# Kernel optimization log

Hardware: AMD Instinct MI355X
Metric: run time of the kernel (lower is better)

The kernel has to match this reference:

```python
import jax, jax.numpy as jnp
import numpy as np

DIM = 1024
H = 16
HD = DIM // H
SCALE = HD ** -0.5
EPS = 1e-5


def setup_inputs() -> dict:
    key = jax.random.key(0)
    ks = jax.random.split(key, 12)
    B, S = 4, 1024
    s = 0.02
    return {
        "image_feat": jax.random.normal(ks[0], (B, S, DIM), jnp.float32),
        "waveform_feat": jax.random.normal(ks[1], (B, S, DIM), jnp.float32),
        "Wq_i": jax.random.normal(ks[2], (DIM, DIM), jnp.float32) * s,
        "bq_i": jnp.zeros((DIM,), jnp.float32),
        "Wkv_w": jax.random.normal(ks[3], (DIM, 2 * DIM), jnp.float32) * s,
        "bkv_w": jnp.zeros((2 * DIM,), jnp.float32),
        "Wq_w": jax.random.normal(ks[4], (DIM, DIM), jnp.float32) * s,
        "bq_w": jnp.zeros((DIM,), jnp.float32),
        "Wkv_i": jax.random.normal(ks[5], (DIM, 2 * DIM), jnp.float32) * s,
        "bkv_i": jnp.zeros((2 * DIM,), jnp.float32),
        "Wp": jax.random.normal(ks[6], (2 * DIM, DIM), jnp.float32) * s,
        "bp": jnp.zeros((DIM,), jnp.float32),
        "gamma": jnp.ones((DIM,), jnp.float32),
        "beta": jnp.zeros((DIM,), jnp.float32),
    }


def _heads(x, B, S):
    # (B, S, DIM) -> (B, H, S, HD)
    return x.reshape(B, S, H, HD).transpose(0, 2, 1, 3)


def _cross_attn(q, k, v, clamp):
    # q,k,v: (B, H, S, HD)
    scores = jnp.einsum("bhqd,bhkd->bhqk", q, k) * SCALE
    if clamp:
        scores = jnp.clip(scores, -100.0, 100.0)
    attn = jax.nn.softmax(scores, axis=-1)
    return jnp.einsum("bhqk,bhkd->bhqd", attn, v)


def reference(image_feat, waveform_feat, Wq_i, bq_i, Wkv_w, bkv_w,
              Wq_w, bq_w, Wkv_i, bkv_i, Wp, bp, gamma, beta):
    B, S, _ = image_feat.shape
    # image queries attend to waveform K/V (with clamp)
    q_s = _heads(image_feat @ Wq_i + bq_i, B, S)
    kv_f = (waveform_feat @ Wkv_w + bkv_w).reshape(B, S, 2, H, HD)
    k_f = kv_f[:, :, 0].transpose(0, 2, 1, 3)
    v_f = kv_f[:, :, 1].transpose(0, 2, 1, 3)
    img_att = _cross_attn(q_s, k_f, v_f, clamp=True)
    img_att = img_att.transpose(0, 2, 1, 3).reshape(B, S, DIM)
    # waveform queries attend to image K/V (no clamp, as in source)
    q_f = _heads(waveform_feat @ Wq_w + bq_w, B, S)
    kv_s = (image_feat @ Wkv_i + bkv_i).reshape(B, S, 2, H, HD)
    k_s = kv_s[:, :, 0].transpose(0, 2, 1, 3)
    v_s = kv_s[:, :, 1].transpose(0, 2, 1, 3)
    wav_att = _cross_attn(q_f, k_s, v_s, clamp=False)
    wav_att = wav_att.transpose(0, 2, 1, 3).reshape(B, S, DIM)
    fused = jnp.concatenate([img_att, wav_att], axis=-1)
    out = fused @ Wp + bp
    # LayerNorm over last dim
    mu = jnp.mean(out, axis=-1, keepdims=True)
    var = jnp.var(out, axis=-1, keepdims=True)
    out = (out - mu) * jax.lax.rsqrt(var + EPS) * gamma + beta
    return out
```

## Files before the change

### kernel.cpp

```cpp
#include <hip/hip_runtime.h>
#include <hip/hip_bf16.h>

#define DEVINL __device__ __forceinline__

typedef float f32x4 __attribute__((ext_vector_type(4)));
typedef __bf16 bf16x8 __attribute__((ext_vector_type(8)));

DEVINL void gld_lds16(const void* g, void* l) {
  __builtin_amdgcn_global_load_lds(
      (const __attribute__((address_space(1))) unsigned int*)g,
      (__attribute__((address_space(3))) unsigned int*)l, 16, 0, 0);
}

DEVINL unsigned short f2bf(float f) {
  __bf16 h = (__bf16)f;
  return __builtin_bit_cast(unsigned short, h);
}

DEVINL f32x4 mfma16(bf16x8 a, bf16x8 b, f32x4 c) {
  return __builtin_amdgcn_mfma_f32_16x16x32_bf16(a, b, c, 0, 0, 0);
}

DEVINL void swz3(int& bn, int& bm, int& z) {
  int gx = gridDim.x, gy = gridDim.y;
  int nwg = gx * gy * gridDim.z;
  int flat = blockIdx.x + gx * (blockIdx.y + gy * blockIdx.z);
  int wg = (flat & 7) * (nwg >> 3) + (flat >> 3);
  bn = wg % gx;
  int t = wg / gx;
  bm = t % gy;
  z = t / gy;
}

__global__ __launch_bounds__(256) void cvt2_kernel(const float* __restrict__ inA,
                                                   unsigned short* __restrict__ outA,
                                                   const float* __restrict__ inB,
                                                   unsigned short* __restrict__ outB) {
  int bx = blockIdx.x;
  const float* in = bx < 4096 ? inA : inB;
  unsigned short* outp = bx < 4096 ? outA : outB;
  int i = (bx & 4095) * 256 + threadIdx.x;
  float4 v = ((const float4*)in)[i];
  ushort4 o;
  o.x = f2bf(v.x); o.y = f2bf(v.y); o.z = f2bf(v.z); o.w = f2bf(v.w);
  ((ushort4*)outp)[i] = o;
}

struct TransArgs {
  const float* W[5];
  unsigned short* Wt[5];
};

DEVINL void trans_tile(const float* W, unsigned short* Wt, int K, int N,
                       int xt, int yt) {
  __shared__ float t[32][33];
  int n0 = xt * 32, k0 = yt * 32;
  int tx = threadIdx.x & 31, ty = threadIdx.x >> 5;
#pragma unroll
  for (int i = 0; i < 4; i++)
    t[ty + i * 8][tx] = W[(size_t)(k0 + ty + i * 8) * N + n0 + tx];
  __syncthreads();
#pragma unroll
  for (int i = 0; i < 4; i++) {
    int n = ty + i * 8;
    Wt[(size_t)(n0 + n) * K + k0 + tx] = f2bf(t[tx][n]);
  }
}

__global__ __launch_bounds__(256) void transpose_all(TransArgs a) {
  int t = blockIdx.x;
  if (t < 1024)       trans_tile(a.W[0], a.Wt[0], 1024, 1024, t % 32, t / 32);
  else if (t < 3072)  { int l = t - 1024; trans_tile(a.W[1], a.Wt[1], 1024, 2048, l % 64, l / 64); }
  else if (t < 4096)  { int l = t - 3072; trans_tile(a.W[2], a.Wt[2], 1024, 1024, l % 32, l / 32); }
  else if (t < 6144)  { int l = t - 4096; trans_tile(a.W[3], a.Wt[3], 1024, 2048, l % 64, l / 64); }
  else                { int l = t - 6144; trans_tile(a.W[4], a.Wt[4], 2048, 1024, l % 32, l / 32); }
}

template <int BM, int BN, int MREP, int NREP>
DEVINL void g256_main(const unsigned short* A, const unsigned short* Bt, int K,
                      int bm, int bn, unsigned short* Al, unsigned short* Bl,
                      f32x4 (&acc)[MREP][NREP]) {
  const int tid = threadIdx.x;
  const int wave = tid >> 6, lane = tid & 63;
  const int lr = lane & 15;
  const int lk16 = (lane >> 4) * 16;
  const int wm = wave >> 2, wn = wave & 3;
  const int swz = (lr & 7) << 4;
  const int nk = K >> 6;
  const size_t Kb = (size_t)K * 2;

#pragma unroll
  for (int m = 0; m < MREP; m++)
#pragma unroll
    for (int n = 0; n < NREP; n++) acc[m][n] = f32x4{0.f, 0.f, 0.f, 0.f};

  auto stage = [&](int buf, int kt) {
#pragma unroll
    for (int i = 0; i < BM / 64; i++) {
      int chunk = i * 512 + tid;
      int row = chunk >> 3, cb = (chunk & 7) * 16;
      const char* src = (const char*)A + (size_t)(bm * BM + row) * Kb +
                        kt * 128 + (cb ^ ((row & 7) << 4));
      char* dst = (char*)(Al + (size_t)buf * BM * 64) + (i * 512 + wave * 64) * 16;
      gld_lds16(src, dst);
    }
#pragma unroll
    for (int i = 0; i < BN / 64; i++) {
      int chunk = i * 512 + tid;
      int row = chunk >> 3, cb = (chunk & 7) * 16;
      const char* src = (const char*)Bt + (size_t)(bn * BN + row) * Kb +
                        kt * 128 + (cb ^ ((row & 7) << 4));
      char* dst = (char*)(Bl + (size_t)buf * BN * 64) + (i * 512 + wave * 64) * 16;
      gld_lds16(src, dst);
    }
  };

  stage(0, 0);
  for (int kt = 0; kt < nk; ++kt) {
    __syncthreads();
    if (kt + 1 < nk) stage((kt + 1) & 1, kt + 1);
    const char* ab = (const char*)(Al + (size_t)(kt & 1) * BM * 64);
    const char* bb = (const char*)(Bl + (size_t)(kt & 1) * BN * 64);
#pragma unroll
    for (int kk = 0; kk < 2; kk++) {
      bf16x8 af[MREP], bf[NREP];
#pragma unroll
      for (int m = 0; m < MREP; m++) {
        int row = wm * (BM / 2) + m * 16 + lr;
        af[m] = *(const bf16x8*)(ab + row * 128 + ((kk * 64 + lk16) ^ swz));
      }
#pragma unroll
      for (int n = 0; n < NREP; n++) {
        int row = wn * (BN / 4) + n * 16 + lr;
        bf[n] = *(const bf16x8*)(bb + row * 128 + ((kk * 64 + lk16) ^ swz));
      }
#pragma unroll
      for (int m = 0; m < MREP; m++)
#pragma unroll
        for (int n = 0; n < NREP; n++)
          acc[m][n] = mfma16(af[m], bf[n], acc[m][n]);
    }
  }
}

__global__ __launch_bounds__(512, 2) void gemm_q2(const unsigned short* __restrict__ A0,
                                                  const unsigned short* __restrict__ B0,
                                                  const float* __restrict__ bias0,
                                                  unsigned short* __restrict__ C0,
                                                  const unsigned short* __restrict__ A1,
                                                  const unsigned short* __restrict__ B1,
                                                  const float* __restrict__ bias1,
                                                  unsigned short* __restrict__ C1) {
  __shared__ unsigned short Al[2 * 256 * 64];
  __shared__ unsigned short Bl[2 * 128 * 64];
  int bn, bm, z;
  swz3(bn, bm, z);
  const unsigned short* A = z ? A1 : A0;
  const unsigned short* Bt = z ? B1 : B0;
  const float* bias = z ? bias1 : bias0;
  unsigned short* C = z ? C1 : C0;
  const int lane = threadIdx.x & 63, wave = threadIdx.x >> 6;
  const int lr = lane & 15, g4 = lane >> 4;
  const int wm = wave >> 2, wn = wave & 3;
  f32x4 acc[8][2];
  g256_main<256, 128, 8, 2>(A, Bt, 1024, bm, bn, Al, Bl, acc);
#pragma unroll
  for (int n = 0; n < 2; n++) {
    int col = bn * 128 + wn * 32 + n * 16 + lr;
    float bv = bias[col];
#pragma unroll
    for (int m = 0; m < 8; m++) {
      int row0 = bm * 256 + wm * 128 + m * 16 + g4 * 4;
#pragma unroll
      for (int r = 0; r < 4; r++)
        C[(size_t)(row0 + r) * 1024 + col] = f2bf((acc[m][n][r] + bv) * 0.125f);
    }
  }
}

__global__ __launch_bounds__(512, 4) void gemm_kv2(const unsigned short* __restrict__ A0,
                                                   const unsigned short* __restrict__ B0,
                                                   const float* __restrict__ bias0,
                                                   unsigned short* __restrict__ K0,
                                                   unsigned short* __restrict__ V0,
                                                   const unsigned short* __restrict__ A1,
                                                   const unsigned short* __restrict__ B1,
                                                   const float* __restrict__ bias1,
                                                   unsigned short* __restrict__ K1,
                                                   unsigned short* __restrict__ V1) {
  __shared__ unsigned short Al[2 * 128 * 64];
  __shared__ unsigned short Bl[2 * 128 * 64];
  int bn, bm, z;
  swz3(bn, bm, z);
  const unsigned short* A = z ? A1 : A0;
  const unsigned short* Bt = z ? B1 : B0;
  const float* bias = z ? bias1 : bias0;
  unsigned short* Kbuf = z ? K1 : K0;
  unsigned short* VtG = z ? V1 : V0;
  const int lane = threadIdx.x & 63, wave = threadIdx.x >> 6;
  const int lr = lane & 15, g4 = lane >> 4;
  const int wm = wave >> 2, wn = wave & 3;
  f32x4 acc[4][2];
  g256_main<128, 128, 4, 2>(A, Bt, 1024, bm, bn, Al, Bl, acc);
#pragma unroll
  for (int n = 0; n < 2; n++) {
    int col = bn * 128 + wn * 32 + n * 16 + lr;
    float bv = bias[col];
#pragma unroll
    for (int m = 0; m < 4; m++) {
      int row0 = bm * 128 + wm * 64 + m * 16 + g4 * 4;
      if (col < 1024) {
#pragma unroll
        for (int r = 0; r < 4; r++)
          Kbuf[(size_t)(row0 + r) * 1024 + col] = f2bf(acc[m][n][r] + bv);
      } else {
        int h = (col - 1024) >> 6, d = (col - 1024) & 63;
        int b = row0 >> 10, s = row0 & 1023;
        ushort4 pk;
        pk.x = f2bf(acc[m][n][0] + bv);
        pk.y = f2bf(acc[m][n][1] + bv);
        pk.z = f2bf(acc[m][n][2] + bv);
        pk.w = f2bf(acc[m][n][3] + bv);
        *(ushort4*)&VtG[((size_t)(b * 16 + h) * 64 + d) * 1024 + s] = pk;
      }
    }
  }
}

__global__ __launch_bounds__(512, 4) void gemm_out(const unsigned short* __restrict__ A,
                                                   const unsigned short* __restrict__ Bt,
                                                   const float* __restrict__ bias,
                                                   float* __restrict__ C) {
  __shared__ unsigned short Al[2 * 128 * 64];
  __shared__ unsigned short Bl[2 * 128 * 64];
  int bn, bm, z;
  swz3(bn, bm, z);
  const int lane = threadIdx.x & 63, wave = threadIdx.x >> 6;
  const int lr = lane & 15, g4 = lane >> 4;
  const int wm = wave >> 2, wn = wave & 3;
  f32x4 acc[4][2];
  g256_main<128, 128, 4, 2>(A, Bt, 2048, bm, bn, Al, Bl, acc);
#pragma unroll
  for (int n = 0; n < 2; n++) {
    int col = bn * 128 + wn * 32 + n * 16 + lr;
    float bv = bias[col];
#pragma unroll
    for (int m = 0; m < 4; m++) {
      int row0 = bm * 128 + wm * 64 + m * 16 + g4 * 4;
#pragma unroll
      for (int r = 0; r < 4; r++)
        C[(size_t)(row0 + r) * 1024 + col] = acc[m][n][r] + bv;
    }
  }
  (void)z;
}

__global__ __launch_bounds__(256, 4) void attn_fused(const unsigned short* __restrict__ Qs,
                                                     const unsigned short* __restrict__ Ks,
                                                     const unsigned short* __restrict__ Vs,
                                                     const unsigned short* __restrict__ Qf,
                                                     const unsigned short* __restrict__ Kf,
                                                     const unsigned short* __restrict__ Vf,
                                                     unsigned short* __restrict__ Out) {
  __shared__ unsigned short Kl[2][64 * 64];
  __shared__ unsigned short Vt[2][64 * 64];
  __shared__ unsigned short Pl[4][16 * 64];

  const int tid = threadIdx.x;
  const int wave = tid >> 6, lane = tid & 63;
  const int qt = blockIdx.y & 7;
  const int u = blockIdx.x + (blockIdx.y >> 3) * 16;
  const int dir = u >> 6, bh = u & 63;
  const int b = bh >> 4, h = bh & 15;
  const unsigned short* Q = dir ? Qf : Qs;
  const unsigned short* Kg = dir ? Kf : Ks;
  const unsigned short* VtG = dir ? Vf : Vs;
  const int outColBase = dir ? 1024 : 0;
  const bool doClamp = (dir == 0);

  const int q16 = lane & 15;
  const int g4 = lane >> 4;
  const int lk16 = g4 * 16;

  bf16x8 qa[2][2];
#pragma unroll
  for (int g = 0; g < 2; g++) {
    const size_t qrow = (size_t)b * 1024 + qt * 128 + wave * 32 + g * 16 + q16;
    const char* qp = (const char*)(Q + qrow * 1024 + h * 64);
    qa[g][0] = *(const bf16x8*)(qp + lk16);
    qa[g][1] = *(const bf16x8*)(qp + 64 + lk16);
  }

  f32x4 acc[2][4] = {};
  float mrun[2] = {-1e30f, -1e30f}, lsum[2] = {0.f, 0.f};

  const char* kbase = (const char*)Kg + (size_t)b * 1024 * 2048 + h * 128;
  const char* vbase = (const char*)VtG + (size_t)bh * 64 * 2048;

  auto stage = [&](int buf, int kt) {
#pragma unroll
    for (int p2 = 0; p2 < 2; p2++) {
      int chunk = tid + p2 * 256;
      int r = chunk >> 3, cb = (chunk & 7) * 16;
      const char* src = kbase + (size_t)(kt * 64 + r) * 2048 + (cb ^ ((r & 7) << 4));
      char* dst = (char*)&Kl[buf][0] + (p2 * 256 + wave * 64) * 16;
      gld_lds16(src, dst);
    }
#pragma unroll
    for (int p2 = 0; p2 < 2; p2++) {
      int chunk = tid + p2 * 256;
      int d = chunk >> 3, ko = (chunk & 7) * 16;
      const char* src = vbase + (size_t)d * 2048 + kt * 128 + (ko ^ ((d & 7) << 4));
      char* dst = (char*)&Vt[buf][0] + (p2 * 256 + wave * 64) * 16;
      gld_lds16(src, dst);
    }
  };

  char* pb = (char*)&Pl[wave][0];

  stage(0, 0);
  for (int kt = 0; kt < 16; ++kt) {
    __syncthreads();
    if (kt < 15) stage((kt + 1) & 1, kt + 1);
    const char* kb = (const char*)&Kl[kt & 1][0];
    const char* vb = (const char*)&Vt[kt & 1][0];

#pragma unroll
    for (int g = 0; g < 2; g++) {
      f32x4 st[4];
#pragma unroll
      for (int t4 = 0; t4 < 4; t4++) {
        int krow = t4 * 16 + q16;
        int sw = (krow & 7) << 4;
        const char* kr = kb + krow * 128;
        bf16x8 kb0 = *(const bf16x8*)(kr + ((0 + lk16) ^ sw));
        bf16x8 kb1 = *(const bf16x8*)(kr + ((64 + lk16) ^ sw));
        f32x4 s = {};
        s = mfma16(kb0, qa[g][0], s);
        s = mfma16(kb1, qa[g][1], s);
        if (doClamp) {
#pragma unroll
          for (int r = 0; r < 4; r++)
            s[r] = fminf(fmaxf(s[r], -100.f), 100.f);
        }
        st[t4] = s;
      }

      float mx = fmaxf(fmaxf(fmaxf(st[0][0], st[0][1]), fmaxf(st[0][2], st[0][3])),
                       fmaxf(fmaxf(st[1][0], st[1][1]), fmaxf(st[1][2], st[1][3])));
      float mx2 = fmaxf(fmaxf(fmaxf(st[2][0], st[2][1]), fmaxf(st[2][2], st[2][3])),
                        fmaxf(fmaxf(st[3][0], st[3][1]), fmaxf(st[3][2], st[3][3])));
      mx = fmaxf(mx, mx2);
      mx = fmaxf(mx, __shfl_xor(mx, 16, 64));
      mx = fmaxf(mx, __shfl_xor(mx, 32, 64));

      if (!__all(mx <= mrun[g] + 8.f)) {
        float mnew = fmaxf(mrun[g], mx);
        float al = __expf(mrun[g] - mnew);
        mrun[g] = mnew;
        lsum[g] *= al;
        float alr[4];
#pragma unroll
        for (int r = 0; r < 4; r++) alr[r] = __shfl(al, 4 * g4 + r, 64);
#pragma unroll
        for (int n = 0; n < 4; n++)
#pragma unroll
          for (int r = 0; r < 4; r++) acc[g][n][r] *= alr[r];
      }
      const float m = mrun[g];
      float sum = 0.f;
#pragma unroll
      for (int t4 = 0; t4 < 4; t4++) {
#pragma unroll
        for (int r = 0; r < 4; r++) {
          float pv = __expf(st[t4][r] - m);
          st[t4][r] = pv;
          sum += pv;
        }
      }
      sum += __shfl_xor(sum, 16, 64);
      sum += __shfl_xor(sum, 32, 64);
      lsum[g] += sum;

#pragma unroll
      for (int t4 = 0; t4 < 4; t4++) {
        unsigned plo = ((unsigned)f2bf(st[t4][1]) << 16) | f2bf(st[t4][0]);
        unsigned phi = ((unsigned)f2bf(st[t4][3]) << 16) | f2bf(st[t4][2]);
        uint2 w2 = {plo, phi};
        *(uint2*)(pb + q16 * 128 + ((t4 * 32 + g4 * 8) ^ ((q16 & 7) << 4))) = w2;
      }

      bf16x8 pa[2];
#pragma unroll
      for (int kc = 0; kc < 2; kc++)
        pa[kc] = *(const bf16x8*)(pb + ((q16 * 128 + kc * 64 + lk16) ^ ((q16 & 7) << 4)));

#pragma unroll
      for (int n = 0; n < 4; n++) {
        int vr = n * 16 + q16;
        int sw = (vr & 7) << 4;
        const char* vp = vb + vr * 128;
#pragma unroll
        for (int kc = 0; kc < 2; kc++) {
          bf16x8 vbv = *(const bf16x8*)(vp + ((kc * 64 + lk16) ^ sw));
          acc[g][n] = mfma16(pa[kc], vbv, acc[g][n]);
        }
      }
    }
  }

#pragma unroll
  for (int g = 0; g < 2; g++) {
    float lr4[4];
#pragma unroll
    for (int r = 0; r < 4; r++) lr4[r] = __shfl(lsum[g], 4 * g4 + r, 64);
    const size_t orow0 = (size_t)b * 1024 + qt * 128 + wave * 32 + g * 16 + g4 * 4;
#pragma unroll
    for (int n = 0; n < 4; n++) {
      int col = outColBase + h * 64 + n * 16 + q16;
#pragma unroll
      for (int r = 0; r < 4; r++) {
        float o = acc[g][n][r] / lr4[r];
        Out[(orow0 + r) * 2048 + col] = f2bf(o);
      }
    }
  }
}

__global__ __launch_bounds__(256) void ln_inplace(float* __restrict__ io,
                                                  const float* __restrict__ gamma,
                                                  const float* __restrict__ beta) {
  __shared__ float red[8];
  int row = blockIdx.x, tid = threadIdx.x;
  float* p = io + (size_t)row * 1024;
  float4 x = ((const float4*)p)[tid];
  float s = x.x + x.y + x.z + x.w;
  float s2 = x.x * x.x + x.y * x.y + x.z * x.z + x.w * x.w;
#pragma unroll
  for (int off = 32; off; off >>= 1) {
    s += __shfl_down(s, off, 64);
    s2 += __shfl_down(s2, off, 64);
  }
  int wv = tid >> 6;
  if ((tid & 63) == 0) { red[wv] = s; red[4 + wv] = s2; }
  __syncthreads();
  if (tid == 0) {
    red[0] = red[0] + red[1] + red[2] + red[3];
    red[4] = red[4] + red[5] + red[6] + red[7];
  }
  __syncthreads();
  float mu = red[0] * (1.f / 1024.f);
  float var = red[4] * (1.f / 1024.f) - mu * mu;
  float inv = rsqrtf(var + 1e-5f);
  float4 g = ((const float4*)gamma)[tid];
  float4 bb = ((const float4*)beta)[tid];
  x.x = (x.x - mu) * inv * g.x + bb.x;
  x.y = (x.y - mu) * inv * g.y + bb.y;
  x.z = (x.z - mu) * inv * g.z + bb.z;
  x.w = (x.w - mu) * inv * g.w + bb.w;
  ((float4*)p)[tid] = x;
}

extern "C" void kernel_launch(void* const* d_in, const int* in_sizes, int n_in,
                              void* d_out, int out_size, void* d_ws, size_t ws_size,
                              hipStream_t stream) {
  (void)in_sizes; (void)n_in; (void)out_size; (void)ws_size;
  const float* image = (const float*)d_in[0];
  const float* wavef = (const float*)d_in[1];
  const float* Wq_i  = (const float*)d_in[2];
  const float* bq_i  = (const float*)d_in[3];
  const float* Wkv_w = (const float*)d_in[4];
  const float* bkv_w = (const float*)d_in[5];
  const float* Wq_w  = (const float*)d_in[6];
  const float* bq_w  = (const float*)d_in[7];
  const float* Wkv_i = (const float*)d_in[8];
  const float* bkv_i = (const float*)d_in[9];
  const float* Wp    = (const float*)d_in[10];
  const float* bp    = (const float*)d_in[11];
  const float* gamma = (const float*)d_in[12];
  const float* beta  = (const float*)d_in[13];
  float* out = (float*)d_out;

  char* ws = (char*)d_ws;
  unsigned short* Xi = (unsigned short*)ws;
  unsigned short* Xw = (unsigned short*)ws + 4096ull * 1024;
  unsigned short* fused = (unsigned short*)ws;
  size_t off = 16ull << 20;
  auto take = [&](size_t bytes) { void* p = ws + off; off += bytes; return p; };
  unsigned short* Wt_qi  = (unsigned short*)take(2ull << 20);
  unsigned short* Wt_kvw = (unsigned short*)take(4ull << 20);
  unsigned short* Wt_qw  = (unsigned short*)take(2ull << 20);
  unsigned short* Wt_kvi = (unsigned short*)take(4ull << 20);
  unsigned short* Wt_p   = (unsigned short*)take(4ull << 20);
  unsigned short* q_s    = (unsigned short*)take(8ull << 20);
  unsigned short* q_f    = (unsigned short*)take(8ull << 20);
  unsigned short* kvK_w  = (unsigned short*)take(8ull << 20);
  unsigned short* VtG_w  = (unsigned short*)take(8ull << 20);
  unsigned short* kvK_s  = (unsigned short*)take(8ull << 20);
  unsigned short* VtG_s  = (unsigned short*)take(8ull << 20);

  cvt2_kernel<<<8192, 256, 0, stream>>>(image, Xi, wavef, Xw);
  TransArgs ta;
  ta.W[0] = Wq_i;  ta.Wt[0] = Wt_qi;
  ta.W[1] = Wkv_w; ta.Wt[1] = Wt_kvw;
  ta.W[2] = Wq_w;  ta.Wt[2] = Wt_qw;
  ta.W[3] = Wkv_i; ta.Wt[3] = Wt_kvi;
  ta.W[4] = Wp;    ta.Wt[4] = Wt_p;
  transpose_all<<<8192, 256, 0, stream>>>(ta);
  gemm_q2<<<dim3(8, 16, 2), 512, 0, stream>>>(Xi, Wt_qi, bq_i, q_s,
                                              Xw, Wt_qw, bq_w, q_f);
  gemm_kv2<<<dim3(16, 32, 2), 512, 0, stream>>>(Xw, Wt_kvw, bkv_w, kvK_w, VtG_w,
                                                Xi, Wt_kvi, bkv_i, kvK_s, VtG_s);
  attn_fused<<<dim3(16, 64), 256, 0, stream>>>(q_s, kvK_w, VtG_w,
                                               q_f, kvK_s, VtG_s, fused);
  gemm_out<<<dim3(8, 32), 512, 0, stream>>>(fused, Wt_p, bp, out);
  ln_inplace<<<4096, 256, 0, stream>>>(out, gamma, beta);
}
```

Baseline: 199.3 us.

## Merge prep and projection kernels, shrink output GEMM tile, add MFMA priority hints

The bf16 input conversion and weight transposes now run in a single prep kernel. The Q and KV projection GEMMs are merged into one 3-slice launch that uses a uniform 128x128 tile, so there are fewer launches and tails. The output projection GEMM switches to 128x64 tiles, doubling its grid for better CU occupancy. The attention kernel wraps its MFMA blocks in s_setprio and moves the clamp out of the score loop, which may help overlap between waves but changes the instruction schedule.

```diff
diff --git a/kernel.cpp b/kernel.cpp
--- a/kernel.cpp
+++ b/kernel.cpp
@@ -32,21 +32,9 @@
   z = t / gy;
 }
 
-__global__ __launch_bounds__(256) void cvt2_kernel(const float* __restrict__ inA,
-                                                   unsigned short* __restrict__ outA,
-                                                   const float* __restrict__ inB,
-                                                   unsigned short* __restrict__ outB) {
-  int bx = blockIdx.x;
-  const float* in = bx < 4096 ? inA : inB;
-  unsigned short* outp = bx < 4096 ? outA : outB;
-  int i = (bx & 4095) * 256 + threadIdx.x;
-  float4 v = ((const float4*)in)[i];
-  ushort4 o;
-  o.x = f2bf(v.x); o.y = f2bf(v.y); o.z = f2bf(v.z); o.w = f2bf(v.w);
-  ((ushort4*)outp)[i] = o;
-}
-
-struct TransArgs {
+struct PrepArgs {
+  const float* inA; unsigned short* outA;
+  const float* inB; unsigned short* outB;
   const float* W[5];
   unsigned short* Wt[5];
 };
@@ -67,8 +55,19 @@
   }
 }
 
-__global__ __launch_bounds__(256) void transpose_all(TransArgs a) {
+__global__ __launch_bounds__(256) void prep_all(PrepArgs a) {
   int t = blockIdx.x;
+  if (t < 8192) {
+    const float* in = t < 4096 ? a.inA : a.inB;
+    unsigned short* outp = t < 4096 ? a.outA : a.outB;
+    int i = (t & 4095) * 256 + threadIdx.x;
+    float4 v = ((const float4*)in)[i];
+    ushort4 o;
+    o.x = f2bf(v.x); o.y = f2bf(v.y); o.z = f2bf(v.z); o.w = f2bf(v.w);
+    ((ushort4*)outp)[i] = o;
+    return;
+  }
+  t -= 8192;
   if (t < 1024)       trans_tile(a.W[0], a.Wt[0], 1024, 1024, t % 32, t / 32);
   else if (t < 3072)  { int l = t - 1024; trans_tile(a.W[1], a.Wt[1], 1024, 2048, l % 64, l / 64); }
   else if (t < 4096)  { int l = t - 3072; trans_tile(a.W[2], a.Wt[2], 1024, 1024, l % 32, l / 32); }
@@ -143,94 +142,16 @@
   }
 }
 
-__global__ __launch_bounds__(512, 2) void gemm_q2(const unsigned short* __restrict__ A0,
-                                                  const unsigned short* __restrict__ B0,
-                                                  const float* __restrict__ bias0,
-                                                  unsigned short* __restrict__ C0,
-                                                  const unsigned short* __restrict__ A1,
-                                                  const unsigned short* __restrict__ B1,
-                                                  const float* __restrict__ bias1,
-                                                  unsigned short* __restrict__ C1) {
-  __shared__ unsigned short Al[2 * 256 * 64];
-  __shared__ unsigned short Bl[2 * 128 * 64];
-  int bn, bm, z;
-  swz3(bn, bm, z);
-  const unsigned short* A = z ? A1 : A0;
-  const unsigned short* Bt = z ? B1 : B0;
-  const float* bias = z ? bias1 : bias0;
-  unsigned short* C = z ? C1 : C0;
-  const int lane = threadIdx.x & 63, wave = threadIdx.x >> 6;
-  const int lr = lane & 15, g4 = lane >> 4;
-  const int wm = wave >> 2, wn = wave & 3;
-  f32x4 acc[8][2];
-  g256_main<256, 128, 8, 2>(A, Bt, 1024, bm, bn, Al, Bl, acc);
-#pragma unroll
-  for (int n = 0; n < 2; n++) {
-    int col = bn * 128 + wn * 32 + n * 16 + lr;
-    float bv = bias[col];
-#pragma unroll
-    for (int m = 0; m < 8; m++) {
-      int row0 = bm * 256 + wm * 128 + m * 16 + g4 * 4;
-#pragma unroll
-      for (int r = 0; r < 4; r++)
-        C[(size_t)(row0 + r) * 1024 + col] = f2bf((acc[m][n][r] + bv) * 0.125f);
-    }
-  }
-}
-
-__global__ __launch_bounds__(512, 4) void gemm_kv2(const unsigned short* __restrict__ A0,
-                                                   const unsigned short* __restrict__ B0,
-                                                   const float* __restrict__ bias0,
-                                                   unsigned short* __restrict__ K0,
-                                                   unsigned short* __restrict__ V0,
-                                                   const unsigned short* __restrict__ A1,
-                                                   const unsigned short* __restrict__ B1,
-                                                   const float* __restrict__ bias1,
-                                                   unsigned short* __restrict__ K1,
-                                                   unsigned short* __restrict__ V1) {
-  __shared__ unsigned short Al[2 * 128 * 64];
-  __shared__ unsigned short Bl[2 * 128 * 64];
-  int bn, bm, z;
-  swz3(bn, bm, z);
-  const unsigned short* A = z ? A1 : A0;
-  const unsigned short* Bt = z ? B1 : B0;
-  const float* bias = z ? bias1 : bias0;
-  unsigned short* Kbuf = z ? K1 : K0;
-  unsigned short* VtG = z ? V1 : V0;
-  const int lane = threadIdx.x & 63, wave = threadIdx.x >> 6;
-  const int lr = lane & 15, g4 = lane >> 4;
-  const int wm = wave >> 2, wn = wave & 3;
-  f32x4 acc[4][2];
-  g256_main<128, 128, 4, 2>(A, Bt, 1024, bm, bn, Al, Bl, acc);
-#pragma unroll
-  for (int n = 0; n < 2; n++) {
-    int col = bn * 128 + wn * 32 + n * 16 + lr;
-    float bv = bias[col];
-#pragma unroll
-    for (int m = 0; m < 4; m++) {
-      int row0 = bm * 128 + wm * 64 + m * 16 + g4 * 4;
-      if (col < 1024) {
-#pragma unroll
-        for (int r = 0; r < 4; r++)
-          Kbuf[(size_t)(row0 + r) * 1024 + col] = f2bf(acc[m][n][r] + bv);
-      } else {
-        int h = (col - 1024) >> 6, d = (col - 1024) & 63;
-        int b = row0 >> 10, s = row0 & 1023;
-        ushort4 pk;
-        pk.x = f2bf(acc[m][n][0] + bv);
-        pk.y = f2bf(acc[m][n][1] + bv);
-        pk.z = f2bf(acc[m][n][2] + bv);
-        pk.w = f2bf(acc[m][n][3] + bv);
-        *(ushort4*)&VtG[((size_t)(b * 16 + h) * 64 + d) * 1024 + s] = pk;
-      }
-    }
-  }
-}
-
-__global__ __launch_bounds__(512, 4) void gemm_out(const unsigned short* __restrict__ A,
-                                                   const unsigned short* __restrict__ Bt,
-                                                   const float* __restrict__ bias,
-                                                   float* __restrict__ C) {
+__global__ __launch_bounds__(512, 4) void gemm_proj(
+    const unsigned short* __restrict__ Xi, const unsigned short* __restrict__ Xw,
+    const unsigned short* __restrict__ Wt_qi, const float* __restrict__ bq_i,
+    unsigned short* __restrict__ q_s,
+    const unsigned short* __restrict__ Wt_qw, const float* __restrict__ bq_w,
+    unsigned short* __restrict__ q_f,
+    const unsigned short* __restrict__ Wt_kvw, const float* __restrict__ bkv_w,
+    unsigned short* __restrict__ K_w, unsigned short* __restrict__ V_w,
+    const unsigned short* __restrict__ Wt_kvi, const float* __restrict__ bkv_i,
+    unsigned short* __restrict__ K_s, unsigned short* __restrict__ V_s) {
   __shared__ unsigned short Al[2 * 128 * 64];
   __shared__ unsigned short Bl[2 * 128 * 64];
   int bn, bm, z;
@@ -239,18 +160,81 @@
   const int lr = lane & 15, g4 = lane >> 4;
   const int wm = wave >> 2, wn = wave & 3;
   f32x4 acc[4][2];
-  g256_main<128, 128, 4, 2>(A, Bt, 2048, bm, bn, Al, Bl, acc);
-#pragma unroll
-  for (int n = 0; n < 2; n++) {
-    int col = bn * 128 + wn * 32 + n * 16 + lr;
-    float bv = bias[col];
-#pragma unroll
-    for (int m = 0; m < 4; m++) {
-      int row0 = bm * 128 + wm * 64 + m * 16 + g4 * 4;
-#pragma unroll
-      for (int r = 0; r < 4; r++)
-        C[(size_t)(row0 + r) * 1024 + col] = acc[m][n][r] + bv;
-    }
+
+  if (z == 2) {
+    const bool isS = bn < 8;
+    const unsigned short* A = isS ? Xi : Xw;
+    const unsigned short* Bt = isS ? Wt_qi : Wt_qw;
+    const float* bias = isS ? bq_i : bq_w;
+    unsigned short* C = isS ? q_s : q_f;
+    const int bq = bn & 7;
+    g256_main<128, 128, 4, 2>(A, Bt, 1024, bm, bq, Al, Bl, acc);
+#pragma unroll
+    for (int n = 0; n < 2; n++) {
+      int col = bq * 128 + wn * 32 + n * 16 + lr;
+      float bv = bias[col];
+#pragma unroll
+      for (int m = 0; m < 4; m++) {
+        int row0 = bm * 128 + wm * 64 + m * 16 + g4 * 4;
+#pragma unroll
+        for (int r = 0; r < 4; r++)
+          C[(size_t)(row0 + r) * 1024 + col] = f2bf((acc[m][n][r] + bv) * 0.125f);
+      }
+    }
+  } else {
+    const unsigned short* A = z ? Xi : Xw;
+    const unsigned short* Bt = z ? Wt_kvi : Wt_kvw;
+    const float* bias = z ? bkv_i : bkv_w;
+    unsigned short* Kbuf = z ? K_s : K_w;
+    unsigned short* VtG = z ? V_s : V_w;
+    g256_main<128, 128, 4, 2>(A, Bt, 1024, bm, bn, Al, Bl, acc);
+#pragma unroll
+    for (int n = 0; n < 2; n++) {
+      int col = bn * 128 + wn * 32 + n * 16 + lr;
+      float bv = bias[col];
+#pragma unroll
+      for (int m = 0; m < 4; m++) {
+        int row0 = bm * 128 + wm * 64 + m * 16 + g4 * 4;
+        if (col < 1024) {
+#pragma unroll
+          for (int r = 0; r < 4; r++)
+            Kbuf[(size_t)(row0 + r) * 1024 + col] = f2bf(acc[m][n][r] + bv);
+        } else {
+          int h = (col - 1024) >> 6, d = (col - 1024) & 63;
+          int b = row0 >> 10, s = row0 & 1023;
+          ushort4 pk;
+          pk.x = f2bf(acc[m][n][0] + bv);
+          pk.y = f2bf(acc[m][n][1] + bv);
+          pk.z = f2bf(acc[m][n][2] + bv);
+          pk.w = f2bf(acc[m][n][3] + bv);
+          *(ushort4*)&VtG[((size_t)(b * 16 + h) * 64 + d) * 1024 + s] = pk;
+        }
+      }
+    }
+  }
+}
+
+__global__ __launch_bounds__(512, 4) void gemm_out(const unsigned short* __restrict__ A,
+                                                   const unsigned short* __restrict__ Bt,
+                                                   const float* __restrict__ bias,
+                                                   float* __restrict__ C) {
+  __shared__ unsigned short Al[2 * 128 * 64];
+  __shared__ unsigned short Bl[2 * 64 * 64];
+  int bn, bm, z;
+  swz3(bn, bm, z);
+  const int lane = threadIdx.x & 63, wave = threadIdx.x >> 6;
+  const int lr = lane & 15, g4 = lane >> 4;
+  const int wm = wave >> 2, wn = wave & 3;
+  f32x4 acc[4][1];
+  g256_main<128, 64, 4, 1>(A, Bt, 2048, bm, bn, Al, Bl, acc);
+  int col = bn * 64 + wn * 16 + lr;
+  float bv = bias[col];
+#pragma unroll
+  for (int m = 0; m < 4; m++) {
+    int row0 = bm * 128 + wm * 64 + m * 16 + g4 * 4;
+#pragma unroll
+    for (int r = 0; r < 4; r++)
+      C[(size_t)(row0 + r) * 1024 + col] = acc[m][0][r] + bv;
   }
   (void)z;
 }
@@ -328,6 +312,7 @@
 #pragma unroll
     for (int g = 0; g < 2; g++) {
       f32x4 st[4];
+      __builtin_amdgcn_s_setprio(1);
 #pragma unroll
       for (int t4 = 0; t4 < 4; t4++) {
         int krow = t4 * 16 + q16;
@@ -338,12 +323,15 @@
         f32x4 s = {};
         s = mfma16(kb0, qa[g][0], s);
         s = mfma16(kb1, qa[g][1], s);
-        if (doClamp) {
+        st[t4] = s;
+      }
+      __builtin_amdgcn_s_setprio(0);
+      if (doClamp) {
+#pragma unroll
+        for (int t4 = 0; t4 < 4; t4++)
 #pragma unroll
           for (int r = 0; r < 4; r++)
-            s[r] = fminf(fmaxf(s[r], -100.f), 100.f);
-        }
-        st[t4] = s;
+            st[t4][r] = fminf(fmaxf(st[t4][r], -100.f), 100.f);
       }
 
       float mx = fmaxf(fmaxf(fmaxf(st[0][0], st[0][1]), fmaxf(st[0][2], st[0][3])),
@@ -395,6 +383,7 @@
       for (int kc = 0; kc < 2; kc++)
         pa[kc] = *(const bf16x8*)(pb + ((q16 * 128 + kc * 64 + lk16) ^ ((q16 & 7) << 4)));
 
+      __builtin_amdgcn_s_setprio(1);
 #pragma unroll
       for (int n = 0; n < 4; n++) {
         int vr = n * 16 + q16;
@@ -406,6 +395,7 @@
           acc[g][n] = mfma16(pa[kc], vbv, acc[g][n]);
         }
       }
+      __builtin_amdgcn_s_setprio(0);
     }
   }
 
@@ -499,20 +489,20 @@
   unsigned short* kvK_s  = (unsigned short*)take(8ull << 20);
   unsigned short* VtG_s  = (unsigned short*)take(8ull << 20);
 
-  cvt2_kernel<<<8192, 256, 0, stream>>>(image, Xi, wavef, Xw);
-  TransArgs ta;
-  ta.W[0] = Wq_i;  ta.Wt[0] = Wt_qi;
-  ta.W[1] = Wkv_w; ta.Wt[1] = Wt_kvw;
-  ta.W[2] = Wq_w;  ta.Wt[2] = Wt_qw;
-  ta.W[3] = Wkv_i; ta.Wt[3] = Wt_kvi;
-  ta.W[4] = Wp;    ta.Wt[4] = Wt_p;
-  transpose_all<<<8192, 256, 0, stream>>>(ta);
-  gemm_q2<<<dim3(8, 16, 2), 512, 0, stream>>>(Xi, Wt_qi, bq_i, q_s,
-                                              Xw, Wt_qw, bq_w, q_f);
-  gemm_kv2<<<dim3(16, 32, 2), 512, 0, stream>>>(Xw, Wt_kvw, bkv_w, kvK_w, VtG_w,
-                                                Xi, Wt_kvi, bkv_i, kvK_s, VtG_s);
+  PrepArgs pa;
+  pa.inA = image; pa.outA = Xi;
+  pa.inB = wavef; pa.outB = Xw;
+  pa.W[0] = Wq_i;  pa.Wt[0] = Wt_qi;
+  pa.W[1] = Wkv_w; pa.Wt[1] = Wt_kvw;
+  pa.W[2] = Wq_w;  pa.Wt[2] = Wt_qw;
+  pa.W[3] = Wkv_i; pa.Wt[3] = Wt_kvi;
+  pa.W[4] = Wp;    pa.Wt[4] = Wt_p;
+  prep_all<<<16384, 256, 0, stream>>>(pa);
+  gemm_proj<<<dim3(16, 32, 3), 512, 0, stream>>>(
+      Xi, Xw, Wt_qi, bq_i, q_s, Wt_qw, bq_w, q_f,
+      Wt_kvw, bkv_w, kvK_w, VtG_w, Wt_kvi, bkv_i, kvK_s, VtG_s);
   attn_fused<<<dim3(16, 64), 256, 0, stream>>>(q_s, kvK_w, VtG_w,
                                                q_f, kvK_s, VtG_s, fused);
-  gemm_out<<<dim3(8, 32), 512, 0, stream>>>(fused, Wt_p, bp, out);
+  gemm_out<<<dim3(16, 32), 512, 0, stream>>>(fused, Wt_p, bp, out);
   ln_inplace<<<4096, 256, 0, stream>>>(out, gamma, beta);
 }
```

Result: faster. 174.4 us (-12.5%).
